# Kernel tuning notes

Hardware: AMD Instinct MI355X
Metric: run time of the kernel (lower is better)

## Reference

```python
import jax, jax.numpy as jnp
import numpy as np

EMBED_DIM = 1024
NUM_HEADS = 16
HEAD_DIM = EMBED_DIM // NUM_HEADS
LN_EPS = 1e-5


def setup_inputs() -> dict:
    key = jax.random.key(0)
    ks = jax.random.split(key, 7)
    B, N, D = 4, 2048, EMBED_DIM
    s = 1.0 / np.sqrt(D)  # ~kaiming-uniform scale for Linear weights
    return {
        "inputs": jax.random.normal(ks[0], (B, N, D), dtype=jnp.float32),
        "W_q": jax.random.uniform(ks[1], (D, D), jnp.float32, -s, s),
        "W_k": jax.random.uniform(ks[2], (D, D), jnp.float32, -s, s),
        "W_v": jax.random.uniform(ks[3], (D, D), jnp.float32, -s, s),
        "W_o": jax.random.uniform(ks[4], (D, D), jnp.float32, -s, s),
        "ln_gamma": jnp.ones((D,), jnp.float32),
        "ln_beta": jnp.zeros((D,), jnp.float32),
    }


def reference(inputs, W_q, W_k, W_v, W_o, ln_gamma, ln_beta):
    x = inputs
    B, N, D = x.shape
    H, Hd = NUM_HEADS, HEAD_DIM
    # torch nn.Linear computes x @ W.T; W_* stored as (out, in)
    q = (x @ W_q.T).reshape(B, N, H, Hd).transpose(0, 2, 1, 3)  # [B,H,N,Hd]
    k = (x @ W_k.T).reshape(B, N, H, Hd).transpose(0, 2, 1, 3)
    v = (x @ W_v.T).reshape(B, N, H, Hd).transpose(0, 2, 1, 3)
    scores = jnp.einsum("bhqd,bhkd->bhqk", q, k) / jnp.sqrt(jnp.float32(Hd))
    attn = jax.nn.softmax(scores, axis=-1)  # dropout p=0 -> identity
    out = jnp.einsum("bhqk,bhkd->bhqd", attn, v)
    out = out.transpose(0, 2, 1, 3).reshape(B, N, D)
    out = out @ W_o.T
    # residual + LayerNorm
    y = out + x
    mu = jnp.mean(y, axis=-1, keepdims=True)
    var = jnp.mean(jnp.square(y - mu), axis=-1, keepdims=True)
    y = (y - mu) * jax.lax.rsqrt(var + LN_EPS)
    return y * ln_gamma + ln_beta
```

## Files before the change

kernel.cpp:

```cpp
#include <hip/hip_runtime.h>
#include <hip/hip_bf16.h>
#include <stdint.h>

typedef __attribute__((ext_vector_type(8))) short bf16x8;
typedef __attribute__((ext_vector_type(4))) float f32x4;

#define GLOBAL_AS __attribute__((address_space(1)))
#define LDS_AS    __attribute__((address_space(3)))

__device__ __forceinline__ void load_lds16(const void* g, void* l) {
  __builtin_amdgcn_global_load_lds((const GLOBAL_AS void*)g, (LDS_AS void*)l, 16, 0, 0);
}

__device__ __forceinline__ short f2bfn(float f) {
  __hip_bfloat16 h = __float2bfloat16(f);
  return __builtin_bit_cast(short, h);
}

__global__ __launch_bounds__(256) void cvt_all(const float* __restrict__ x,
                                               const float* __restrict__ q,
                                               const float* __restrict__ k,
                                               const float* __restrict__ v,
                                               const float* __restrict__ o,
                                               short* __restrict__ xb,
                                               short* __restrict__ Wb,
                                               short* __restrict__ Wob) {
  const int bid = blockIdx.x;
  const float* src;
  short* dst;
  int i;
  if (bid < 4096) {
    src = x; dst = xb; i = (bid * 256 + threadIdx.x) * 8;
  } else {
    const int sel = (bid - 4096) >> 9;
    const int inner = (bid - 4096) & 511;
    i = (inner * 256 + threadIdx.x) * 8;
    src = sel == 0 ? q : sel == 1 ? k : sel == 2 ? v : o;
    dst = sel == 0 ? Wb : sel == 1 ? Wb + 1024 * 1024
        : sel == 2 ? Wb + 2 * 1024 * 1024 : Wob;
  }
  float4 a = *(const float4*)(src + i);
  float4 b = *(const float4*)(src + i + 4);
  bf16x8 ov;
  ov[0] = f2bfn(a.x); ov[1] = f2bfn(a.y); ov[2] = f2bfn(a.z); ov[3] = f2bfn(a.w);
  ov[4] = f2bfn(b.x); ov[5] = f2bfn(b.y); ov[6] = f2bfn(b.z); ov[7] = f2bfn(b.w);
  *(bf16x8*)(dst + i) = ov;
}

__global__ __launch_bounds__(256) void gemm_qkvt(const short* __restrict__ xb,
                                                 const short* __restrict__ Wqk,
                                                 const short* __restrict__ Wv,
                                                 short* __restrict__ qkv,
                                                 short* __restrict__ VT) {
  __shared__ short As[128 * 64];
  __shared__ short Bs[128 * 64];
  const int t = threadIdx.x, l = t & 63, w = t >> 6;
  const int g = l >> 4, li = l & 15;
  const int wr = w >> 1, wc = w & 1;
  const int bid = blockIdx.x;
  const bool isqk = bid < 1024;
  const short* A;
  const short* B;
  int bm, bn;
  if (isqk) {
    A = xb; B = Wqk;
    bm = (bid & 7) * 8 + ((bid >> 3) & 7);
    bn = bid >> 6;
  } else {
    const int b2 = bid - 1024;
    A = Wv; B = xb;
    bm = b2 & 7;
    bn = b2 >> 3;
  }
  const int sw = li & 7;
  const int K = 1024;
  f32x4 acc[4][4] = {};
  const size_t arow0 = (size_t)(bm * 128) * K;
  const size_t brow0 = (size_t)(bn * 128) * K;
  for (int k0 = 0; k0 < K; k0 += 64) {
    __syncthreads();
#pragma unroll
    for (int it = 0; it < 4; ++it) {
      int e = it * 2048 + t * 8;
      int r = e >> 6;
      int cs = (e >> 3) & 7;
      int cg = cs ^ (r & 7);
      load_lds16(A + arow0 + (size_t)r * K + (k0 + cg * 8), &As[e]);
      load_lds16(B + brow0 + (size_t)r * K + (k0 + cg * 8), &Bs[e]);
    }
    __syncthreads();
#pragma unroll
    for (int kk = 0; kk < 2; ++kk) {
      bf16x8 af[4], bfr[4];
#pragma unroll
      for (int m = 0; m < 4; ++m)
        af[m] = *(const bf16x8*)&As[(wr * 64 + m * 16 + li) * 64 + (((kk * 4 + g) ^ sw) * 8)];
#pragma unroll
      for (int n = 0; n < 4; ++n)
        bfr[n] = *(const bf16x8*)&Bs[(wc * 64 + n * 16 + li) * 64 + (((kk * 4 + g) ^ sw) * 8)];
#pragma unroll
      for (int m = 0; m < 4; ++m)
#pragma unroll
        for (int n = 0; n < 4; ++n)
          acc[m][n] = __builtin_amdgcn_mfma_f32_16x16x32_bf16(af[m], bfr[n], acc[m][n], 0, 0, 0);
    }
  }
#pragma unroll
  for (int m = 0; m < 4; ++m)
#pragma unroll
    for (int n = 0; n < 4; ++n)
#pragma unroll
      for (int r = 0; r < 4; ++r) {
        int row = bm * 128 + wr * 64 + m * 16 + g * 4 + r;
        int col = bn * 128 + wc * 64 + n * 16 + li;
        if (isqk)
          qkv[(size_t)row * 3072 + col] = f2bfn(acc[m][n][r]);
        else
          VT[(size_t)(col >> 11) * (1024 * 2048) + (size_t)row * 2048 +
             (col & 2047)] = f2bfn(acc[m][n][r]);
      }
}

__global__ __launch_bounds__(256) void gemm_proj(const short* __restrict__ A,
                                                 const short* __restrict__ B,
                                                 float* __restrict__ Cp) {
  __shared__ short As[128 * 64];
  __shared__ short Bs[128 * 64];
  const int t = threadIdx.x, l = t & 63, w = t >> 6;
  const int g = l >> 4, li = l & 15;
  const int wr = w >> 1, wc = w & 1;
  const int bid = blockIdx.x;
  const int bm = (bid & 7) * 8 + ((bid >> 3) & 7);
  const int bn = bid >> 6;
  const int sw = li & 7;
  const int K = 1024;
  f32x4 acc[4][4] = {};
  const size_t arow0 = (size_t)(bm * 128) * K;
  const size_t brow0 = (size_t)(bn * 128) * K;
  for (int k0 = 0; k0 < K; k0 += 64) {
    __syncthreads();
#pragma unroll
    for (int it = 0; it < 4; ++it) {
      int e = it * 2048 + t * 8;
      int r = e >> 6;
      int cs = (e >> 3) & 7;
      int cg = cs ^ (r & 7);
      load_lds16(A + arow0 + (size_t)r * K + (k0 + cg * 8), &As[e]);
      load_lds16(B + brow0 + (size_t)r * K + (k0 + cg * 8), &Bs[e]);
    }
    __syncthreads();
#pragma unroll
    for (int kk = 0; kk < 2; ++kk) {
      bf16x8 af[4], bfr[4];
#pragma unroll
      for (int m = 0; m < 4; ++m)
        af[m] = *(const bf16x8*)&As[(wr * 64 + m * 16 + li) * 64 + (((kk * 4 + g) ^ sw) * 8)];
#pragma unroll
      for (int n = 0; n < 4; ++n)
        bfr[n] = *(const bf16x8*)&Bs[(wc * 64 + n * 16 + li) * 64 + (((kk * 4 + g) ^ sw) * 8)];
#pragma unroll
      for (int m = 0; m < 4; ++m)
#pragma unroll
        for (int n = 0; n < 4; ++n)
          acc[m][n] = __builtin_amdgcn_mfma_f32_16x16x32_bf16(af[m], bfr[n], acc[m][n], 0, 0, 0);
    }
  }
#pragma unroll
  for (int m = 0; m < 4; ++m)
#pragma unroll
    for (int n = 0; n < 4; ++n)
#pragma unroll
      for (int r = 0; r < 4; ++r) {
        int row = bm * 128 + wr * 64 + m * 16 + g * 4 + r;
        int col = bn * 128 + wc * 64 + n * 16 + li;
        Cp[(size_t)row * 1024 + col] = acc[m][n][r];
      }
}

__global__ __launch_bounds__(512, 4) void attn_fwd(const short* __restrict__ qkv,
                                                   const short* __restrict__ VT,
                                                   short* __restrict__ obuf) {
  const int f0 = blockIdx.x;
  const int work = (f0 & 7) * 64 + (f0 >> 3);
  const int qt = work & 7;
  const int bh = work >> 3;
  const int b = bh >> 4, h = bh & 15;
  const int t = threadIdx.x, w = t >> 6, l = t & 63;
  const int g = l >> 4, li = l & 15;

  __shared__ short Ks[2][64 * 64];
  __shared__ short Vts[2][64 * 64];
  __shared__ short Ps[8][2][16 * 64];

  const size_t base = (size_t)b * 2048 * 3072 + (size_t)h * 64;
  const short* Vsrc = VT + (size_t)bh * 64 * 2048;

  bf16x8 qf[2][2];
  {
    const float QSC = 0.125f * 1.44269504088896341f;
#pragma unroll
    for (int qh = 0; qh < 2; ++qh) {
      const short* qp = qkv + base + (size_t)(qt * 256 + w * 32 + qh * 16 + li) * 3072;
#pragma unroll
      for (int c = 0; c < 2; ++c) {
        bf16x8 v = *(const bf16x8*)(qp + c * 32 + g * 8);
#pragma unroll
        for (int i = 0; i < 8; ++i) {
          float f = __uint_as_float(((unsigned)(unsigned short)v[i]) << 16);
          v[i] = f2bfn(f * QSC);
        }
        qf[qh][c] = v;
      }
    }
  }

  bf16x8 ones;
#pragma unroll
  for (int i = 0; i < 8; ++i) ones[i] = (short)0x3F80;

  f32x4 o_[2][4], lacc[2];
#pragma unroll
  for (int qh = 0; qh < 2; ++qh) {
#pragma unroll
    for (int dj = 0; dj < 4; ++dj) o_[qh][dj] = (f32x4){0.f, 0.f, 0.f, 0.f};
    lacc[qh] = (f32x4){0.f, 0.f, 0.f, 0.f};
  }

  const int sw = li & 7;

#define STAGE(buf, kt_)                                                          \
  {                                                                              \
    int e = t * 8;                                                               \
    int r = e >> 6;                                                              \
    int cs = (e >> 3) & 7;                                                       \
    int cg = cs ^ (r & 7);                                                       \
    load_lds16(qkv + base + 1024 + (size_t)((kt_) * 64 + r) * 3072 + cg * 8,     \
               &Ks[buf][e]);                                                     \
    load_lds16(Vsrc + (size_t)r * 2048 + (kt_) * 64 + cg * 8, &Vts[buf][e]);     \
  }

  STAGE(0, 0);
  asm volatile("s_waitcnt vmcnt(0)" ::: "memory");
  __syncthreads();

  for (int kt = 0; kt < 32; ++kt) {
    const int cur = kt & 1;
    if (kt + 1 < 32) STAGE(cur ^ 1, kt + 1);

    f32x4 s_[2][4];
#pragma unroll
    for (int qh = 0; qh < 2; ++qh)
#pragma unroll
      for (int j = 0; j < 4; ++j) s_[qh][j] = (f32x4){0.f, 0.f, 0.f, 0.f};
    __builtin_amdgcn_s_setprio(1);
#pragma unroll
    for (int c = 0; c < 2; ++c)
#pragma unroll
      for (int j = 0; j < 4; ++j) {
        bf16x8 kf = *(const bf16x8*)&Ks[cur][(j * 16 + li) * 64 + (((c * 4 + g) ^ sw) * 8)];
        s_[0][j] = __builtin_amdgcn_mfma_f32_16x16x32_bf16(kf, qf[0][c], s_[0][j], 0, 0, 0);
        s_[1][j] = __builtin_amdgcn_mfma_f32_16x16x32_bf16(kf, qf[1][c], s_[1][j], 0, 0, 0);
      }
    __builtin_amdgcn_s_setprio(0);

#pragma unroll
    for (int qh = 0; qh < 2; ++qh) {
#pragma unroll
      for (int j = 0; j < 4; ++j) {
        float p0 = exp2f(s_[qh][j][0]);
        float p1 = exp2f(s_[qh][j][1]);
        float p2 = exp2f(s_[qh][j][2]);
        float p3 = exp2f(s_[qh][j][3]);
        unsigned u0, u1;
        asm("v_cvt_pk_bf16_f32 %0, %1, %2" : "=v"(u0) : "v"(p0), "v"(p1));
        asm("v_cvt_pk_bf16_f32 %0, %1, %2" : "=v"(u1) : "v"(p2), "v"(p3));
        uint2 pk2; pk2.x = u0; pk2.y = u1;
        int pos = (j * 16 + g * 4) ^ (sw << 3);
        *(uint2*)&Ps[w][qh][li * 64 + pos] = pk2;
      }
    }
    asm volatile("s_waitcnt lgkmcnt(0)" ::: "memory");

    __builtin_amdgcn_s_setprio(1);
#pragma unroll
    for (int c = 0; c < 2; ++c) {
      bf16x8 vb[4];
#pragma unroll
      for (int dj = 0; dj < 4; ++dj)
        vb[dj] = *(const bf16x8*)&Vts[cur][(dj * 16 + li) * 64 + (((c * 4 + g) ^ sw) * 8)];
#pragma unroll
      for (int qh = 0; qh < 2; ++qh) {
        bf16x8 pa = *(const bf16x8*)&Ps[w][qh][li * 64 + (((c * 4 + g) ^ sw) * 8)];
        lacc[qh] = __builtin_amdgcn_mfma_f32_16x16x32_bf16(pa, ones, lacc[qh], 0, 0, 0);
#pragma unroll
        for (int dj = 0; dj < 4; ++dj)
          o_[qh][dj] = __builtin_amdgcn_mfma_f32_16x16x32_bf16(pa, vb[dj], o_[qh][dj], 0, 0, 0);
      }
    }
    __builtin_amdgcn_s_setprio(0);

    asm volatile("s_waitcnt vmcnt(0)" ::: "memory");
    __syncthreads();
  }

#pragma unroll
  for (int qh = 0; qh < 2; ++qh)
#pragma unroll
    for (int r = 0; r < 4; ++r) {
      float ilr = 1.f / lacc[qh][r];
      int row = b * 2048 + qt * 256 + w * 32 + qh * 16 + g * 4 + r;
#pragma unroll
      for (int dj = 0; dj < 4; ++dj) {
        int col = h * 64 + dj * 16 + li;
        obuf[(size_t)row * 1024 + col] = f2bfn(o_[qh][dj][r] * ilr);
      }
    }
#undef STAGE
}

__global__ __launch_bounds__(256) void resid_ln(const float* __restrict__ U,
                                                const float* __restrict__ x,
                                                const float* __restrict__ gamma,
                                                const float* __restrict__ beta,
                                                float* __restrict__ out) {
  const int row = blockIdx.x;
  const int t = threadIdx.x, w = t >> 6, l = t & 63;
  const float4 uu = *(const float4*)(U + (size_t)row * 1024 + t * 4);
  const float4 xx = *(const float4*)(x + (size_t)row * 1024 + t * 4);
  float y[4] = {uu.x + xx.x, uu.y + xx.y, uu.z + xx.z, uu.w + xx.w};
  float s = (y[0] + y[1]) + (y[2] + y[3]);
#pragma unroll
  for (int d = 1; d < 64; d <<= 1) s += __shfl_xor(s, d);
  __shared__ float red[4];
  if (l == 0) red[w] = s;
  __syncthreads();
  s = red[0] + red[1] + red[2] + red[3];
  const float mu = s * (1.f / 1024.f);
  float vs = 0.f;
#pragma unroll
  for (int i = 0; i < 4; ++i) { float d0 = y[i] - mu; vs += d0 * d0; }
#pragma unroll
  for (int d = 1; d < 64; d <<= 1) vs += __shfl_xor(vs, d);
  __syncthreads();
  if (l == 0) red[w] = vs;
  __syncthreads();
  vs = red[0] + red[1] + red[2] + red[3];
  const float rstd = rsqrtf(vs * (1.f / 1024.f) + 1e-5f);
  const float4 gg = *(const float4*)(gamma + t * 4);
  const float4 bb = *(const float4*)(beta + t * 4);
  float4 oo;
  oo.x = (y[0] - mu) * rstd * gg.x + bb.x;
  oo.y = (y[1] - mu) * rstd * gg.y + bb.y;
  oo.z = (y[2] - mu) * rstd * gg.z + bb.z;
  oo.w = (y[3] - mu) * rstd * gg.w + bb.w;
  *(float4*)(out + (size_t)row * 1024 + t * 4) = oo;
}

extern "C" void kernel_launch(void* const* d_in, const int* in_sizes, int n_in,
                              void* d_out, int out_size, void* d_ws, size_t ws_size,
                              hipStream_t stream) {
  const float* x     = (const float*)d_in[0];
  const float* W_q   = (const float*)d_in[1];
  const float* W_k   = (const float*)d_in[2];
  const float* W_v   = (const float*)d_in[3];
  const float* W_o   = (const float*)d_in[4];
  const float* gamma = (const float*)d_in[5];
  const float* beta  = (const float*)d_in[6];
  float* out = (float*)d_out;

  char* ws = (char*)d_ws;
  short* xb   = (short*)ws;  ws += (size_t)8192 * 1024 * 2;
  short* Wb   = (short*)ws;  ws += (size_t)3072 * 1024 * 2;
  short* Wob  = (short*)ws;  ws += (size_t)1024 * 1024 * 2;
  short* qkv  = (short*)ws;  ws += (size_t)8192 * 3072 * 2;
  short* obuf = (short*)ws;  ws += (size_t)8192 * 1024 * 2;
  float* U    = (float*)ws;  ws += (size_t)8192 * 1024 * 4;
  short* VT   = (short*)U;

  cvt_all<<<6144, 256, 0, stream>>>(x, W_q, W_k, W_v, W_o, xb, Wb, Wob);
  gemm_qkvt<<<1536, 256, 0, stream>>>(xb, Wb, Wb + 2 * 1024 * 1024, qkv, VT);
  attn_fwd<<<512, 512, 0, stream>>>(qkv, VT, obuf);
  gemm_proj<<<512, 256, 0, stream>>>(obuf, Wob, U);
  resid_ln<<<8192, 256, 0, stream>>>(U, x, gamma, beta, out);
}
```

Measured before the change: 219.9 us.

## Use 32x32x16 MFMA in attention with register-resident P and LDS-staged output

Rewrites the attention inner loop to use 32x32x16 bf16 MFMAs with transposed (K·Q^T) scores, so the P tile stays in registers and is reshuffled with v_permlane32_swap instead of round-tripping through per-wave LDS. The row-sum is now accumulated with VALU adds plus a single cross-half shuffle instead of extra MFMAs against a ones vector. The epilogue stages the output through the reused K/V LDS buffers so each lane can issue 16-byte global stores. This removes LDS traffic, the lgkm wait and the redundant MFMAs, at the cost of higher register pressure from the 16-wide accumulators.

```diff
diff --git a/kernel.cpp b/kernel.cpp
--- a/kernel.cpp
+++ b/kernel.cpp
@@ -4,6 +4,8 @@
 
 typedef __attribute__((ext_vector_type(8))) short bf16x8;
 typedef __attribute__((ext_vector_type(4))) float f32x4;
+typedef __attribute__((ext_vector_type(16))) float f32x16;
+typedef __attribute__((ext_vector_type(4))) unsigned u32x4;
 
 #define GLOBAL_AS __attribute__((address_space(1)))
 #define LDS_AS    __attribute__((address_space(3)))
@@ -15,6 +17,9 @@
 __device__ __forceinline__ short f2bfn(float f) {
   __hip_bfloat16 h = __float2bfloat16(f);
   return __builtin_bit_cast(short, h);
+}
+__device__ __forceinline__ float bf2f(short s) {
+  return __uint_as_float(((unsigned)(unsigned short)s) << 16);
 }
 
 __global__ __launch_bounds__(256) void cvt_all(const float* __restrict__ x,
@@ -186,47 +191,33 @@
   const int bh = work >> 3;
   const int b = bh >> 4, h = bh & 15;
   const int t = threadIdx.x, w = t >> 6, l = t & 63;
-  const int g = l >> 4, li = l & 15;
+  const int li = l & 31, hi = l >> 5;
+  const int sw = li & 7;
 
   __shared__ short Ks[2][64 * 64];
   __shared__ short Vts[2][64 * 64];
-  __shared__ short Ps[8][2][16 * 64];
 
   const size_t base = (size_t)b * 2048 * 3072 + (size_t)h * 64;
   const short* Vsrc = VT + (size_t)bh * 64 * 2048;
-
-  bf16x8 qf[2][2];
+  const int qrow0 = qt * 256 + w * 32;
+
+  bf16x8 qf[4];
   {
     const float QSC = 0.125f * 1.44269504088896341f;
-#pragma unroll
-    for (int qh = 0; qh < 2; ++qh) {
-      const short* qp = qkv + base + (size_t)(qt * 256 + w * 32 + qh * 16 + li) * 3072;
-#pragma unroll
-      for (int c = 0; c < 2; ++c) {
-        bf16x8 v = *(const bf16x8*)(qp + c * 32 + g * 8);
-#pragma unroll
-        for (int i = 0; i < 8; ++i) {
-          float f = __uint_as_float(((unsigned)(unsigned short)v[i]) << 16);
-          v[i] = f2bfn(f * QSC);
-        }
-        qf[qh][c] = v;
-      }
-    }
-  }
-
-  bf16x8 ones;
-#pragma unroll
-  for (int i = 0; i < 8; ++i) ones[i] = (short)0x3F80;
-
-  f32x4 o_[2][4], lacc[2];
-#pragma unroll
-  for (int qh = 0; qh < 2; ++qh) {
-#pragma unroll
-    for (int dj = 0; dj < 4; ++dj) o_[qh][dj] = (f32x4){0.f, 0.f, 0.f, 0.f};
-    lacc[qh] = (f32x4){0.f, 0.f, 0.f, 0.f};
-  }
-
-  const int sw = li & 7;
+    const short* qp = qkv + base + (size_t)(qrow0 + li) * 3072;
+#pragma unroll
+    for (int c = 0; c < 4; ++c) {
+      bf16x8 v = *(const bf16x8*)(qp + c * 16 + hi * 8);
+#pragma unroll
+      for (int i = 0; i < 8; ++i) v[i] = f2bfn(bf2f(v[i]) * QSC);
+      qf[c] = v;
+    }
+  }
+
+  f32x16 o0, o1;
+#pragma unroll
+  for (int i = 0; i < 16; ++i) { o0[i] = 0.f; o1[i] = 0.f; }
+  float l_ = 0.f;
 
 #define STAGE(buf, kt_)                                                          \
   {                                                                              \
@@ -247,55 +238,49 @@
     const int cur = kt & 1;
     if (kt + 1 < 32) STAGE(cur ^ 1, kt + 1);
 
-    f32x4 s_[2][4];
-#pragma unroll
-    for (int qh = 0; qh < 2; ++qh)
-#pragma unroll
-      for (int j = 0; j < 4; ++j) s_[qh][j] = (f32x4){0.f, 0.f, 0.f, 0.f};
+    f32x16 s0, s1;
+#pragma unroll
+    for (int i = 0; i < 16; ++i) { s0[i] = 0.f; s1[i] = 0.f; }
     __builtin_amdgcn_s_setprio(1);
 #pragma unroll
-    for (int c = 0; c < 2; ++c)
-#pragma unroll
-      for (int j = 0; j < 4; ++j) {
-        bf16x8 kf = *(const bf16x8*)&Ks[cur][(j * 16 + li) * 64 + (((c * 4 + g) ^ sw) * 8)];
-        s_[0][j] = __builtin_amdgcn_mfma_f32_16x16x32_bf16(kf, qf[0][c], s_[0][j], 0, 0, 0);
-        s_[1][j] = __builtin_amdgcn_mfma_f32_16x16x32_bf16(kf, qf[1][c], s_[1][j], 0, 0, 0);
-      }
+    for (int c = 0; c < 4; ++c) {
+      bf16x8 kf0 = *(const bf16x8*)&Ks[cur][li * 64 + (((c * 2 + hi) ^ sw) * 8)];
+      bf16x8 kf1 = *(const bf16x8*)&Ks[cur][(32 + li) * 64 + (((c * 2 + hi) ^ sw) * 8)];
+      s0 = __builtin_amdgcn_mfma_f32_32x32x16_bf16(kf0, qf[c], s0, 0, 0, 0);
+      s1 = __builtin_amdgcn_mfma_f32_32x32x16_bf16(kf1, qf[c], s1, 0, 0, 0);
+    }
     __builtin_amdgcn_s_setprio(0);
 
-#pragma unroll
-    for (int qh = 0; qh < 2; ++qh) {
-#pragma unroll
-      for (int j = 0; j < 4; ++j) {
-        float p0 = exp2f(s_[qh][j][0]);
-        float p1 = exp2f(s_[qh][j][1]);
-        float p2 = exp2f(s_[qh][j][2]);
-        float p3 = exp2f(s_[qh][j][3]);
-        unsigned u0, u1;
-        asm("v_cvt_pk_bf16_f32 %0, %1, %2" : "=v"(u0) : "v"(p0), "v"(p1));
-        asm("v_cvt_pk_bf16_f32 %0, %1, %2" : "=v"(u1) : "v"(p2), "v"(p3));
-        uint2 pk2; pk2.x = u0; pk2.y = u1;
-        int pos = (j * 16 + g * 4) ^ (sw << 3);
-        *(uint2*)&Ps[w][qh][li * 64 + pos] = pk2;
-      }
-    }
-    asm volatile("s_waitcnt lgkmcnt(0)" ::: "memory");
+    unsigned u0[8], u1[8];
+    float acc = 0.f;
+#pragma unroll
+    for (int m = 0; m < 8; ++m) {
+      float a0 = exp2f(s0[2 * m]);
+      float a1 = exp2f(s0[2 * m + 1]);
+      float b0 = exp2f(s1[2 * m]);
+      float b1 = exp2f(s1[2 * m + 1]);
+      acc += (a0 + a1) + (b0 + b1);
+      asm("v_cvt_pk_bf16_f32 %0, %1, %2" : "=v"(u0[m]) : "v"(a0), "v"(a1));
+      asm("v_cvt_pk_bf16_f32 %0, %1, %2" : "=v"(u1[m]) : "v"(b0), "v"(b1));
+    }
+    l_ += acc;
 
     __builtin_amdgcn_s_setprio(1);
 #pragma unroll
-    for (int c = 0; c < 2; ++c) {
-      bf16x8 vb[4];
-#pragma unroll
-      for (int dj = 0; dj < 4; ++dj)
-        vb[dj] = *(const bf16x8*)&Vts[cur][(dj * 16 + li) * 64 + (((c * 4 + g) ^ sw) * 8)];
-#pragma unroll
-      for (int qh = 0; qh < 2; ++qh) {
-        bf16x8 pa = *(const bf16x8*)&Ps[w][qh][li * 64 + (((c * 4 + g) ^ sw) * 8)];
-        lacc[qh] = __builtin_amdgcn_mfma_f32_16x16x32_bf16(pa, ones, lacc[qh], 0, 0, 0);
-#pragma unroll
-        for (int dj = 0; dj < 4; ++dj)
-          o_[qh][dj] = __builtin_amdgcn_mfma_f32_16x16x32_bf16(pa, vb[dj], o_[qh][dj], 0, 0, 0);
-      }
+    for (int kc = 0; kc < 4; ++kc) {
+      const int cc = kc & 1;
+      unsigned a0 = (kc < 2 ? u0 : u1)[cc * 4 + 0];
+      unsigned a1 = (kc < 2 ? u0 : u1)[cc * 4 + 1];
+      unsigned a2 = (kc < 2 ? u0 : u1)[cc * 4 + 2];
+      unsigned a3 = (kc < 2 ? u0 : u1)[cc * 4 + 3];
+      asm("v_permlane32_swap_b32 %0, %1" : "+v"(a0), "+v"(a2));
+      asm("v_permlane32_swap_b32 %0, %1" : "+v"(a1), "+v"(a3));
+      u32x4 pw; pw[0] = a0; pw[1] = a1; pw[2] = a2; pw[3] = a3;
+      bf16x8 pf = __builtin_bit_cast(bf16x8, pw);
+      bf16x8 vt0 = *(const bf16x8*)&Vts[cur][li * 64 + (((kc * 2 + hi) ^ sw) * 8)];
+      bf16x8 vt1 = *(const bf16x8*)&Vts[cur][(32 + li) * 64 + (((kc * 2 + hi) ^ sw) * 8)];
+      o0 = __builtin_amdgcn_mfma_f32_32x32x16_bf16(vt0, pf, o0, 0, 0, 0);
+      o1 = __builtin_amdgcn_mfma_f32_32x32x16_bf16(vt1, pf, o1, 0, 0, 0);
     }
     __builtin_amdgcn_s_setprio(0);
 
@@ -303,18 +288,26 @@
     __syncthreads();
   }
 
-#pragma unroll
-  for (int qh = 0; qh < 2; ++qh)
-#pragma unroll
-    for (int r = 0; r < 4; ++r) {
-      float ilr = 1.f / lacc[qh][r];
-      int row = b * 2048 + qt * 256 + w * 32 + qh * 16 + g * 4 + r;
-#pragma unroll
-      for (int dj = 0; dj < 4; ++dj) {
-        int col = h * 64 + dj * 16 + li;
-        obuf[(size_t)row * 1024 + col] = f2bfn(o_[qh][dj][r] * ilr);
-      }
-    }
+  l_ += __shfl_xor(l_, 32);
+  const float il = 1.f / l_;
+
+  short* Olds = (w < 4) ? (&Ks[0][0] + w * 2048) : (&Vts[0][0] + (w - 4) * 2048);
+#pragma unroll
+  for (int td = 0; td < 2; ++td) {
+    f32x16 oo = td ? o1 : o0;
+#pragma unroll
+    for (int r = 0; r < 16; ++r) {
+      int d = (r & 3) + 8 * (r >> 2) + 4 * hi + 32 * td;
+      Olds[li * 64 + (d ^ (sw << 3))] = f2bfn(oo[r] * il);
+    }
+  }
+  __syncthreads();
+#pragma unroll
+  for (int j = 0; j < 4; ++j) {
+    int dc = hi * 4 + j;
+    bf16x8 v = *(const bf16x8*)&Olds[li * 64 + ((dc ^ sw) * 8)];
+    *(bf16x8*)(obuf + (size_t)(b * 2048 + qrow0 + li) * 1024 + h * 64 + dc * 8) = v;
+  }
 #undef STAGE
 }
 
```

Result: slower. 225.6 us (+2.6%).
